# Optimization experiments

Hardware: AMD Instinct MI355X
Metric: run time of the kernel (lower is better)

## Reference

```python
import jax, jax.numpy as jnp
import numpy as np

N_NODES = 100000

def _gcn_norm(edge_index, num_nodes):
    # add self-loops, compute symmetric normalization coeffs per edge
    loops = jnp.arange(num_nodes, dtype=edge_index.dtype)
    src = jnp.concatenate([edge_index[0], loops])
    dst = jnp.concatenate([edge_index[1], loops])
    deg = jax.ops.segment_sum(jnp.ones_like(dst, dtype=jnp.float32), dst,
                              num_segments=num_nodes)
    dinv = jnp.where(deg > 0, jax.lax.rsqrt(deg), 0.0)
    norm = dinv[src] * dinv[dst]  # [E + N]
    return src, dst, norm

def _gcn_conv(x, W, b, src, dst, norm, num_nodes):
    h = x @ W                              # [N, out] transform first (PyG order)
    msg = h[src] * norm[:, None]           # gather + scale
    out = jax.ops.segment_sum(msg, dst, num_segments=num_nodes)  # scatter-add
    return out + b

def setup_inputs() -> dict:
    key = jax.random.key(0)
    k1, k2, k3, k4 = jax.random.split(key, 4)
    F_in, H, C = 128, 64, 40
    x = jax.random.normal(k1, (N_NODES, F_in), dtype=jnp.float32)
    edge_index = jax.random.randint(k2, (2, 1600000), 0, N_NODES, dtype=jnp.int64)
    W1 = jax.random.normal(k3, (F_in, H), dtype=jnp.float32) / np.sqrt(F_in)
    b1 = jnp.zeros((H,), dtype=jnp.float32)
    W2 = jax.random.normal(k4, (H, C), dtype=jnp.float32) / np.sqrt(H)
    b2 = jnp.zeros((C,), dtype=jnp.float32)
    return {"x": x, "edge_index": edge_index, "W1": W1, "b1": b1, "W2": W2, "b2": b2}

def reference(x, edge_index, W1, b1, W2, b2):
    num_nodes = x.shape[0]
    src, dst, norm = _gcn_norm(edge_index, num_nodes)
    h = _gcn_conv(x, W1, b1, src, dst, norm, num_nodes)
    h = jax.nn.relu(h)
    # dropout is identity in eval mode (training=False)
    h = _gcn_conv(h, W2, b2, src, dst, norm, num_nodes)
    return jax.nn.log_softmax(h, axis=1)
```

## Files before the change

kernel.cpp:

```cpp
#include <hip/hip_runtime.h>
#include <math.h>

#define NPB 256
#define BSH 8
#define MAXNB 400
#define BIN_CHUNK 8192
#define HIST_CHUNK 16384

typedef __attribute__((ext_vector_type(8))) short bf16x8;
typedef __attribute__((ext_vector_type(4))) float f32x4;
typedef __attribute__((ext_vector_type(2))) float f32x2;

__device__ __forceinline__ unsigned short f2bf(float f){
  unsigned int u = __float_as_uint(f);
  unsigned int r = (u + 0x7FFFu + ((u >> 16) & 1u)) >> 16;
  return (unsigned short)r;
}

__device__ __forceinline__ bf16x8 cvt8(float4 a, float4 b){
  union { unsigned u[4]; bf16x8 v; } r;
  asm("v_cvt_pk_bf16_f32 %0, %1, %2" : "=v"(r.u[0]) : "v"(a.x), "v"(a.y));
  asm("v_cvt_pk_bf16_f32 %0, %1, %2" : "=v"(r.u[1]) : "v"(a.z), "v"(a.w));
  asm("v_cvt_pk_bf16_f32 %0, %1, %2" : "=v"(r.u[2]) : "v"(b.x), "v"(b.y));
  asm("v_cvt_pk_bf16_f32 %0, %1, %2" : "=v"(r.u[3]) : "v"(b.z), "v"(b.w));
  return r.v;
}

__global__ void k_prep(const float* __restrict__ W1, const float* __restrict__ W2,
                       unsigned short* __restrict__ w1t, unsigned short* __restrict__ w2t,
                       int* __restrict__ bcnt, int NB){
  int t = threadIdx.x;
  if(blockIdx.x == 0){
    for(int i = t; i < 8192; i += 256){
      int k = i >> 6, f = i & 63;
      w1t[f*128 + k] = f2bf(W1[i]);
    }
  } else {
    for(int i = t; i < 3072; i += 256){
      int c = i >> 6, k = i & 63;
      w2t[c*64 + k] = (c < 40) ? f2bf(W2[k*40 + c]) : (unsigned short)0;
    }
    for(int i = t; i < NB; i += 256) bcnt[i] = 0;
  }
}


__global__ __launch_bounds__(256) void k_bhist(const int* __restrict__ dst, int E,
                                               int* __restrict__ bcnt, int NB){
  __shared__ int l[MAXNB];
  int t = threadIdx.x;
  int base = blockIdx.x*HIST_CHUNK;
  int end = base + HIST_CHUNK; if(end > E) end = E;
  for(int b = t; b < NB; b += 256) l[b] = 0;
  __syncthreads();
  for(int i = base + t; i < end; i += 256) atomicAdd(&l[dst[i] >> BSH], 1);
  __syncthreads();
  for(int b = t; b < NB; b += 256){ int c = l[b]; if(c) atomicAdd(&bcnt[b], c); }
}

__global__ void k_bscan(const int* __restrict__ bcnt, int* __restrict__ bofs,
                        int* __restrict__ bcur, int NB, int E){
  __shared__ int sh[1024];
  int t = threadIdx.x;
  int c0 = (2*t   < NB) ? bcnt[2*t]   : 0;
  int c1 = (2*t+1 < NB) ? bcnt[2*t+1] : 0;
  sh[t] = c0 + c1; __syncthreads();
  for(int off = 1; off < 1024; off <<= 1){
    int v = (t >= off) ? sh[t - off] : 0;
    __syncthreads();
    sh[t] += v;
    __syncthreads();
  }
  int pairEx = sh[t] - (c0 + c1);
  if(2*t   < NB){ bofs[2*t]   = pairEx;      bcur[2*t]   = pairEx; }
  if(2*t+1 < NB){ bofs[2*t+1] = pairEx + c0; bcur[2*t+1] = pairEx + c0; }
  if(t == 0) bofs[NB] = E;
}

__global__ __launch_bounds__(256) void k_binpass(const int* __restrict__ src,
                          const int* __restrict__ dst, int E,
                          int* __restrict__ bcur, unsigned int* __restrict__ binned, int NB){
  __shared__ int lcnt[MAXNB];
  __shared__ int lpos[MAXNB];
  int t = threadIdx.x;
  int base = blockIdx.x * BIN_CHUNK;
  int end = base + BIN_CHUNK; if(end > E) end = E;
  for(int b = t; b < NB; b += 256) lcnt[b] = 0;
  __syncthreads();
  for(int i = base + t; i < end; i += 256)
    atomicAdd(&lcnt[dst[i] >> BSH], 1);
  __syncthreads();
  for(int b = t; b < NB; b += 256){
    int c = lcnt[b];
    lpos[b] = c ? atomicAdd(&bcur[b], c) : 0;
  }
  __syncthreads();
  for(int i = base + t; i < end; i += 256){
    int d = dst[i];
    int b = d >> BSH;
    unsigned int rec = (unsigned int)src[i] | ((unsigned int)(d & (NPB-1)) << 17);
    int p = atomicAdd(&lpos[b], 1);
    binned[p] = rec;
  }
}

__global__ __launch_bounds__(256) void k_bscatter(const unsigned int* __restrict__ binned,
     const int* __restrict__ bofs, int* __restrict__ csr, int* __restrict__ row_ofs,
     float* __restrict__ dinv, int N, int E, int NB){
  __shared__ int lcnt[NPB];
  __shared__ int lofs[NPB];
  __shared__ int lcur[NPB];
  __shared__ int wsum[4];
  int b = blockIdx.x, t = threadIdx.x;
  int beg = bofs[b], end = bofs[b+1];
  lcnt[t] = 0;
  __syncthreads();
  for(int i = beg + t; i < end; i += 256) atomicAdd(&lcnt[binned[i] >> 17], 1);
  __syncthreads();
  int c = lcnt[t];
  int lane = t & 63, wid = t >> 6;
  int v = c;
  #pragma unroll
  for(int off = 1; off < 64; off <<= 1){
    int nv = __shfl_up(v, off, 64);
    if(lane >= off) v += nv;
  }
  if(lane == 63) wsum[wid] = v;
  __syncthreads();
  int wpre = 0;
  #pragma unroll
  for(int k2 = 0; k2 < 4; k2++) if(k2 < wid) wpre += wsum[k2];
  int ex = wpre + v - c;
  lofs[t] = beg + ex; lcur[t] = 0;
  int node = (b << BSH) + t;
  if(node < N){
    row_ofs[node] = beg + ex;
    dinv[node] = rsqrtf((float)(c + 1));
  }
  __syncthreads();
  for(int i = beg + t; i < end; i += 256){
    unsigned int rec = binned[i];
    int dl = rec >> 17;
    int pos = lofs[dl] + atomicAdd(&lcur[dl], 1);
    csr[pos] = (int)(rec & 0x1FFFFu);
  }
  if(b == NB-1 && t == 0) row_ofs[N] = E;
}

__global__ __launch_bounds__(256) void k_gemm1(const float* __restrict__ x,
                        const unsigned short* __restrict__ w1t,
                        const float* __restrict__ dinv, unsigned int* __restrict__ g1, int n){
  __shared__ unsigned short xs[128*136];
  __shared__ unsigned short wt[64*136];
  int tid = threadIdx.x;
  int nodeBase = blockIdx.x*128;
  for(int i = tid; i < 1024; i += 256){
    int f = i >> 4, seg = i & 15;
    *(uint4*)&wt[f*136 + seg*8] = *(const uint4*)&w1t[f*128 + seg*8];
  }
  {
    const float4* x4 = (const float4*)x;
    for(int i = tid; i < 2048; i += 256){
      int node = i >> 4, seg = i & 15;
      float4 va = make_float4(0.f,0.f,0.f,0.f), vb = va;
      if(nodeBase + node < n){
        va = x4[(size_t)(nodeBase + node)*32 + seg*2];
        vb = x4[(size_t)(nodeBase + node)*32 + seg*2 + 1];
      }
      *(bf16x8*)&xs[node*136 + seg*8] = cvt8(va, vb);
    }
  }
  __syncthreads();

  int w = tid >> 6, lane = tid & 63;
  int ml = lane & 15, q = lane >> 4;
  int n0 = nodeBase + w*32 + ml;
  int n1 = n0 + 16;
  bool vn0 = n0 < n, vn1 = n1 < n;

  f32x4 a00 = {0.f,0.f,0.f,0.f}, a01 = {0.f,0.f,0.f,0.f},
        a02 = {0.f,0.f,0.f,0.f}, a03 = {0.f,0.f,0.f,0.f};
  f32x4 a10 = {0.f,0.f,0.f,0.f}, a11 = {0.f,0.f,0.f,0.f},
        a12 = {0.f,0.f,0.f,0.f}, a13 = {0.f,0.f,0.f,0.f};
  const unsigned short* brow = &xs[(w*32 + ml)*136 + q*8];
  const unsigned short* arow = &wt[ml*136 + q*8];
  #pragma unroll
  for(int s = 0; s < 4; s++){
    bf16x8 bb0 = *(const bf16x8*)(brow +        s*32);
    bf16x8 bb1 = *(const bf16x8*)(brow + 2176 + s*32);
    bf16x8 a0 = *(const bf16x8*)(arow +    0 + s*32);
    bf16x8 a1 = *(const bf16x8*)(arow + 2176 + s*32);
    bf16x8 a2 = *(const bf16x8*)(arow + 4352 + s*32);
    bf16x8 a3 = *(const bf16x8*)(arow + 6528 + s*32);
    a00 = __builtin_amdgcn_mfma_f32_16x16x32_bf16(a0, bb0, a00, 0, 0, 0);
    a01 = __builtin_amdgcn_mfma_f32_16x16x32_bf16(a1, bb0, a01, 0, 0, 0);
    a02 = __builtin_amdgcn_mfma_f32_16x16x32_bf16(a2, bb0, a02, 0, 0, 0);
    a03 = __builtin_amdgcn_mfma_f32_16x16x32_bf16(a3, bb0, a03, 0, 0, 0);
    a10 = __builtin_amdgcn_mfma_f32_16x16x32_bf16(a0, bb1, a10, 0, 0, 0);
    a11 = __builtin_amdgcn_mfma_f32_16x16x32_bf16(a1, bb1, a11, 0, 0, 0);
    a12 = __builtin_amdgcn_mfma_f32_16x16x32_bf16(a2, bb1, a12, 0, 0, 0);
    a13 = __builtin_amdgcn_mfma_f32_16x16x32_bf16(a3, bb1, a13, 0, 0, 0);
  }
  if(vn0){
    float dv = dinv[n0];
    unsigned base16 = ((unsigned)n0 << 4) + q;
    int p;
    p = __builtin_amdgcn_cvt_pk_fp8_f32(a00[0]*dv, a00[1]*dv, 0, false);
    p = __builtin_amdgcn_cvt_pk_fp8_f32(a00[2]*dv, a00[3]*dv, p, true);
    g1[base16 +  0] = (unsigned)p;
    p = __builtin_amdgcn_cvt_pk_fp8_f32(a01[0]*dv, a01[1]*dv, 0, false);
    p = __builtin_amdgcn_cvt_pk_fp8_f32(a01[2]*dv, a01[3]*dv, p, true);
    g1[base16 +  4] = (unsigned)p;
    p = __builtin_amdgcn_cvt_pk_fp8_f32(a02[0]*dv, a02[1]*dv, 0, false);
    p = __builtin_amdgcn_cvt_pk_fp8_f32(a02[2]*dv, a02[3]*dv, p, true);
    g1[base16 +  8] = (unsigned)p;
    p = __builtin_amdgcn_cvt_pk_fp8_f32(a03[0]*dv, a03[1]*dv, 0, false);
    p = __builtin_amdgcn_cvt_pk_fp8_f32(a03[2]*dv, a03[3]*dv, p, true);
    g1[base16 + 12] = (unsigned)p;
  }
  if(vn1){
    float dv = dinv[n1];
    unsigned base16 = ((unsigned)n1 << 4) + q;
    int p;
    p = __builtin_amdgcn_cvt_pk_fp8_f32(a10[0]*dv, a10[1]*dv, 0, false);
    p = __builtin_amdgcn_cvt_pk_fp8_f32(a10[2]*dv, a10[3]*dv, p, true);
    g1[base16 +  0] = (unsigned)p;
    p = __builtin_amdgcn_cvt_pk_fp8_f32(a11[0]*dv, a11[1]*dv, 0, false);
    p = __builtin_amdgcn_cvt_pk_fp8_f32(a11[2]*dv, a11[3]*dv, p, true);
    g1[base16 +  4] = (unsigned)p;
    p = __builtin_amdgcn_cvt_pk_fp8_f32(a12[0]*dv, a12[1]*dv, 0, false);
    p = __builtin_amdgcn_cvt_pk_fp8_f32(a12[2]*dv, a12[3]*dv, p, true);
    g1[base16 +  8] = (unsigned)p;
    p = __builtin_amdgcn_cvt_pk_fp8_f32(a13[0]*dv, a13[1]*dv, 0, false);
    p = __builtin_amdgcn_cvt_pk_fp8_f32(a13[2]*dv, a13[3]*dv, p, true);
    g1[base16 + 12] = (unsigned)p;
  }
}

__global__ __launch_bounds__(256) void k_agg1g2(const unsigned* __restrict__ g1,
    const int* __restrict__ row_ofs, const int* __restrict__ csr,
    const float* __restrict__ dinv, const float* __restrict__ b1,
    const unsigned short* __restrict__ w2t, unsigned char* __restrict__ g2, int n){
  __shared__ unsigned short us[64*72];
  __shared__ unsigned short ws2[48*72];
  int t = threadIdx.x;
  int nodeBase = blockIdx.x*64;
  for(int i = t; i < 384; i += 256){
    int row = i >> 3, seg = i & 7;
    *(uint4*)&ws2[row*72 + seg*8] = *(const uint4*)&w2t[row*64 + seg*8];
  }
  int lane = t & 63;
  int f = lane & 15;
  int bq = (lane & 48) << 2;
  int qg = t >> 4;
  float4 bb1 = ((const float4*)b1)[f];
  #pragma unroll 1
  for(int i = 0; i < 4; i++){
    int node = nodeBase + qg*4 + i;
    int lrow = qg*4 + i;
    if(node < n){
      int beg = row_ofs[node], end = row_ofs[node+1];
      unsigned v = g1[((unsigned)node << 4) + f];
      f32x2 s01 = __builtin_amdgcn_cvt_pk_f32_fp8(v, false);
      f32x2 s23 = __builtin_amdgcn_cvt_pk_f32_fp8(v, true);
      for(int e = beg; e < end; e += 16){
        int rem = end - e; if(rem > 16) rem = 16;
        int idxv = (f < rem) ? csr[e + f] : 0;
        int j = 0;
        for(; j + 4 <= rem; j += 4){
          int r0 = __builtin_amdgcn_ds_bpermute(bq + ((j+0) << 2), idxv);
          int r1 = __builtin_amdgcn_ds_bpermute(bq + ((j+1) << 2), idxv);
          int r2 = __builtin_amdgcn_ds_bpermute(bq + ((j+2) << 2), idxv);
          int r3 = __builtin_amdgcn_ds_bpermute(bq + ((j+3) << 2), idxv);
          unsigned v0 = g1[((unsigned)r0 << 4) + f];
          unsigned v1 = g1[((unsigned)r1 << 4) + f];
          unsigned v2 = g1[((unsigned)r2 << 4) + f];
          unsigned v3 = g1[((unsigned)r3 << 4) + f];
          s01 += __builtin_amdgcn_cvt_pk_f32_fp8(v0, false);
          s23 += __builtin_amdgcn_cvt_pk_f32_fp8(v0, true);
          s01 += __builtin_amdgcn_cvt_pk_f32_fp8(v1, false);
          s23 += __builtin_amdgcn_cvt_pk_f32_fp8(v1, true);
          s01 += __builtin_amdgcn_cvt_pk_f32_fp8(v2, false);
          s23 += __builtin_amdgcn_cvt_pk_f32_fp8(v2, true);
          s01 += __builtin_amdgcn_cvt_pk_f32_fp8(v3, false);
          s23 += __builtin_amdgcn_cvt_pk_f32_fp8(v3, true);
        }
        for(; j < rem; j++){
          int r0 = __builtin_amdgcn_ds_bpermute(bq + (j << 2), idxv);
          unsigned v0 = g1[((unsigned)r0 << 4) + f];
          s01 += __builtin_amdgcn_cvt_pk_f32_fp8(v0, false);
          s23 += __builtin_amdgcn_cvt_pk_f32_fp8(v0, true);
        }
      }
      float dv = dinv[node];
      float h0 = fmaxf(fmaf(dv, s01.x, bb1.x), 0.f);
      float h1 = fmaxf(fmaf(dv, s01.y, bb1.y), 0.f);
      float h2 = fmaxf(fmaf(dv, s23.x, bb1.z), 0.f);
      float h3 = fmaxf(fmaf(dv, s23.y, bb1.w), 0.f);
      unsigned p0, p1;
      asm("v_cvt_pk_bf16_f32 %0, %1, %2" : "=v"(p0) : "v"(dv*h0), "v"(dv*h1));
      asm("v_cvt_pk_bf16_f32 %0, %1, %2" : "=v"(p1) : "v"(dv*h2), "v"(dv*h3));
      *(uint2*)&us[lrow*72 + f*4] = make_uint2(p0, p1);
    } else {
      *(uint2*)&us[lrow*72 + f*4] = make_uint2(0u, 0u);
    }
  }
  __syncthreads();
  int w = t >> 6;
  int ml = lane & 15, q = lane >> 4;
  f32x4 acc0 = {0.f,0.f,0.f,0.f}, acc1 = {0.f,0.f,0.f,0.f}, acc2 = {0.f,0.f,0.f,0.f};
  const unsigned short* brow = &us[(w*16 + ml)*72 + q*8];
  const unsigned short* a0r = &ws2[ml*72 + q*8];
  #pragma unroll
  for(int s = 0; s < 2; s++){
    bf16x8 bb = *(const bf16x8*)(brow + s*32);
    bf16x8 a0 = *(const bf16x8*)(a0r +    0 + s*32);
    bf16x8 a1 = *(const bf16x8*)(a0r + 1152 + s*32);
    bf16x8 a2 = *(const bf16x8*)(a0r + 2304 + s*32);
    acc0 = __builtin_amdgcn_mfma_f32_16x16x32_bf16(a0, bb, acc0, 0, 0, 0);
    acc1 = __builtin_amdgcn_mfma_f32_16x16x32_bf16(a1, bb, acc1, 0, 0, 0);
    acc2 = __builtin_amdgcn_mfma_f32_16x16x32_bf16(a2, bb, acc2, 0, 0, 0);
  }
  int node = nodeBase + w*16 + ml;
  if(node < n){
    unsigned* gd = (unsigned*)g2;
    unsigned rb = (unsigned)node*10u + q;
    int p;
    p = __builtin_amdgcn_cvt_pk_fp8_f32(acc0[0], acc0[1], 0, false);
    p = __builtin_amdgcn_cvt_pk_fp8_f32(acc0[2], acc0[3], p, true);
    gd[rb + 0] = (unsigned)p;
    p = __builtin_amdgcn_cvt_pk_fp8_f32(acc1[0], acc1[1], 0, false);
    p = __builtin_amdgcn_cvt_pk_fp8_f32(acc1[2], acc1[3], p, true);
    gd[rb + 4] = (unsigned)p;
    if(q < 2){
      p = __builtin_amdgcn_cvt_pk_fp8_f32(acc2[0], acc2[1], 0, false);
      p = __builtin_amdgcn_cvt_pk_fp8_f32(acc2[2], acc2[3], p, true);
      gd[rb + 8] = (unsigned)p;
    }
  }
}

__global__ __launch_bounds__(256) void k_agg2(const unsigned char* __restrict__ g2,
     const int* __restrict__ row_ofs, const int* __restrict__ csr,
     const float* __restrict__ dinv, const float* __restrict__ b2,
     float* __restrict__ out, int N){
  int t = threadIdx.x;
  int lane = t & 63;
  int f = lane & 15;
  int fc = (f < 10) ? f : 0;
  int bq = (lane & 48) << 2;
  int node = blockIdx.x*16 + (t >> 4);
  if(node >= N) return;
  int beg = row_ofs[node], end = row_ofs[node+1];
  const unsigned* gd = (const unsigned*)g2;
  unsigned v = gd[(unsigned)node*10u + fc];
  f32x2 s01 = __builtin_amdgcn_cvt_pk_f32_fp8(v, false);
  f32x2 s23 = __builtin_amdgcn_cvt_pk_f32_fp8(v, true);
  for(int e = beg; e < end; e += 16){
    int rem = end - e; if(rem > 16) rem = 16;
    int idxv = (f < rem) ? csr[e + f] : 0;
    int j = 0;
    for(; j + 4 <= rem; j += 4){
      int r0 = __builtin_amdgcn_ds_bpermute(bq + ((j+0) << 2), idxv);
      int r1 = __builtin_amdgcn_ds_bpermute(bq + ((j+1) << 2), idxv);
      int r2 = __builtin_amdgcn_ds_bpermute(bq + ((j+2) << 2), idxv);
      int r3 = __builtin_amdgcn_ds_bpermute(bq + ((j+3) << 2), idxv);
      unsigned v0 = gd[(unsigned)r0*10u + fc];
      unsigned v1 = gd[(unsigned)r1*10u + fc];
      unsigned v2 = gd[(unsigned)r2*10u + fc];
      unsigned v3 = gd[(unsigned)r3*10u + fc];
      s01 += __builtin_amdgcn_cvt_pk_f32_fp8(v0, false);
      s23 += __builtin_amdgcn_cvt_pk_f32_fp8(v0, true);
      s01 += __builtin_amdgcn_cvt_pk_f32_fp8(v1, false);
      s23 += __builtin_amdgcn_cvt_pk_f32_fp8(v1, true);
      s01 += __builtin_amdgcn_cvt_pk_f32_fp8(v2, false);
      s23 += __builtin_amdgcn_cvt_pk_f32_fp8(v2, true);
      s01 += __builtin_amdgcn_cvt_pk_f32_fp8(v3, false);
      s23 += __builtin_amdgcn_cvt_pk_f32_fp8(v3, true);
    }
    for(; j < rem; j++){
      int r0 = __builtin_amdgcn_ds_bpermute(bq + (j << 2), idxv);
      unsigned v0 = gd[(unsigned)r0*10u + fc];
      s01 += __builtin_amdgcn_cvt_pk_f32_fp8(v0, false);
      s23 += __builtin_amdgcn_cvt_pk_f32_fp8(v0, true);
    }
  }
  float dv = dinv[node];
  float4 bb = ((const float4*)b2)[fc];
  float l0 = fmaf(dv, s01.x, bb.x);
  float l1 = fmaf(dv, s01.y, bb.y);
  float l2 = fmaf(dv, s23.x, bb.z);
  float l3 = fmaf(dv, s23.y, bb.w);
  bool valid = (f < 10);
  float m = valid ? fmaxf(fmaxf(l0,l1), fmaxf(l2,l3)) : -INFINITY;
  m = fmaxf(m, __shfl_xor(m,1,64)); m = fmaxf(m, __shfl_xor(m,2,64));
  m = fmaxf(m, __shfl_xor(m,4,64)); m = fmaxf(m, __shfl_xor(m,8,64));
  float ex = valid ? (expf(l0-m)+expf(l1-m)) + (expf(l2-m)+expf(l3-m)) : 0.f;
  ex += __shfl_xor(ex,1,64); ex += __shfl_xor(ex,2,64);
  ex += __shfl_xor(ex,4,64); ex += __shfl_xor(ex,8,64);
  float ll = logf(ex);
  if(valid){
    ((float4*)out)[(unsigned)node*10u + f] = make_float4(l0-m-ll, l1-m-ll, l2-m-ll, l3-m-ll);
  }
}


extern "C" void kernel_launch(void* const* d_in, const int* in_sizes, int n_in,
                              void* d_out, int out_size, void* d_ws, size_t ws_size,
                              hipStream_t stream){
  const float* x  = (const float*)d_in[0];
  const int*   ei = (const int*)  d_in[1];
  const float* W1 = (const float*)d_in[2];
  const float* b1 = (const float*)d_in[3];
  const float* W2 = (const float*)d_in[4];
  const float* b2 = (const float*)d_in[5];
  float* out = (float*)d_out;

  int N = in_sizes[0] / 128;
  int E = in_sizes[1] / 2;
  const int* src = ei;
  const int* dst = ei + E;
  int NB = (N + NPB - 1) >> BSH;

  char* w = (char*)d_ws;
  auto alloc = [&](size_t bytes) -> char* {
    char* p = w;
    w += (bytes + 511) & ~(size_t)511;
    return p;
  };
  int*   bcnt    = (int*)  alloc((size_t)NB*4);
  int*   bofs    = (int*)  alloc((size_t)(NB+1)*4);
  int*   bcur    = (int*)  alloc((size_t)NB*4);
  int*   row_ofs = (int*)  alloc((size_t)(N+1)*4);
  float* dinv    = (float*)alloc((size_t)N*4);
  unsigned int* binned = (unsigned int*)alloc((size_t)E*4);
  int*   csr     = (int*)  alloc((size_t)E*4);
  unsigned int*   g1 = (unsigned int*)  alloc((size_t)N*64);
  unsigned char*  g2 = (unsigned char*) alloc((size_t)N*40);
  unsigned short* w1t = (unsigned short*)alloc((size_t)64*128*2);
  unsigned short* w2t = (unsigned short*)alloc((size_t)48*64*2);

  k_prep    <<<2, 256, 0, stream>>>(W1, W2, w1t, w2t, bcnt, NB);
  k_bhist   <<<(E+HIST_CHUNK-1)/HIST_CHUNK, 256, 0, stream>>>(dst, E, bcnt, NB);
  k_bscan   <<<1, 1024, 0, stream>>>(bcnt, bofs, bcur, NB, E);
  k_binpass <<<(E+BIN_CHUNK-1)/BIN_CHUNK, 256, 0, stream>>>(src, dst, E, bcur, binned, NB);
  k_bscatter<<<NB, 256, 0, stream>>>(binned, bofs, csr, row_ofs, dinv, N, E, NB);

  k_gemm1   <<<(N+127)/128, 256, 0, stream>>>(x, w1t, dinv, g1, N);
  k_agg1g2  <<<(N+63)/64, 256, 0, stream>>>(g1, row_ofs, csr, dinv, b1, w2t, g2, N);
  k_agg2    <<<(N+15)/16, 256, 0, stream>>>(g2, row_ofs, csr, dinv, b2, out, N);
}
```

Before: 228.1 us.

## Gather 8-byte feature chunks with half-wave per node and padded zero sentinel rows

Both aggregation kernels now give each node 8 lanes, each loading 8 fp8 features as a uint2, instead of 16 lanes loading 4 bytes each. Each wave therefore covers twice as many nodes and issues wider, fewer gather loads. Layer-2 features are padded to 64-byte rows, and a zeroed sentinel row at index N lets out-of-range edge slots load harmlessly, which removes the remainder loops. The prep kernel is folded into the histogram launch and replaced by a memset, and the histogram and binning chunk sizes are reduced so more blocks run. The padding increases layer-2 gather bytes, and the fixed 8-wide inner loop does wasted loads on low-degree nodes.

```diff
diff --git a/kernel.cpp b/kernel.cpp
--- a/kernel.cpp
+++ b/kernel.cpp
@@ -4,8 +4,8 @@
 #define NPB 256
 #define BSH 8
 #define MAXNB 400
-#define BIN_CHUNK 8192
-#define HIST_CHUNK 16384
+#define BIN_CHUNK 4096
+#define HIST_CHUNK 4096
 
 typedef __attribute__((ext_vector_type(8))) short bf16x8;
 typedef __attribute__((ext_vector_type(4))) float f32x4;
@@ -26,36 +26,40 @@
   return r.v;
 }
 
-__global__ void k_prep(const float* __restrict__ W1, const float* __restrict__ W2,
-                       unsigned short* __restrict__ w1t, unsigned short* __restrict__ w2t,
-                       int* __restrict__ bcnt, int NB){
-  int t = threadIdx.x;
-  if(blockIdx.x == 0){
-    for(int i = t; i < 8192; i += 256){
-      int k = i >> 6, f = i & 63;
-      w1t[f*128 + k] = f2bf(W1[i]);
-    }
-  } else {
-    for(int i = t; i < 3072; i += 256){
-      int c = i >> 6, k = i & 63;
-      w2t[c*64 + k] = (c < 40) ? f2bf(W2[k*40 + c]) : (unsigned short)0;
-    }
-    for(int i = t; i < NB; i += 256) bcnt[i] = 0;
-  }
-}
-
 
 __global__ __launch_bounds__(256) void k_bhist(const int* __restrict__ dst, int E,
-                                               int* __restrict__ bcnt, int NB){
+                                               int* __restrict__ bcnt, int NB, int NBH,
+                                               const float* __restrict__ W1,
+                                               const float* __restrict__ W2,
+                                               unsigned short* __restrict__ w1t,
+                                               unsigned short* __restrict__ w2t,
+                                               unsigned* __restrict__ g1,
+                                               unsigned* __restrict__ g2d, int N){
   __shared__ int l[MAXNB];
-  int t = threadIdx.x;
-  int base = blockIdx.x*HIST_CHUNK;
+  int t = threadIdx.x, b = blockIdx.x;
+  if(b >= NBH){
+    if(b == NBH){
+      for(int i = t; i < 8192; i += 256){
+        int k = i >> 6, f = i & 63;
+        w1t[f*128 + k] = f2bf(W1[i]);
+      }
+      if(t < 16) g1[((size_t)(unsigned)N << 4) + t] = 0;
+    } else {
+      for(int i = t; i < 3072; i += 256){
+        int c = i >> 6, k = i & 63;
+        w2t[c*64 + k] = (c < 40) ? f2bf(W2[k*40 + c]) : (unsigned short)0;
+      }
+      if(t < 16) g2d[((size_t)(unsigned)N << 4) + t] = 0;
+    }
+    return;
+  }
+  int base = b*HIST_CHUNK;
   int end = base + HIST_CHUNK; if(end > E) end = E;
-  for(int b = t; b < NB; b += 256) l[b] = 0;
+  for(int i = t; i < NB; i += 256) l[i] = 0;
   __syncthreads();
   for(int i = base + t; i < end; i += 256) atomicAdd(&l[dst[i] >> BSH], 1);
   __syncthreads();
-  for(int b = t; b < NB; b += 256){ int c = l[b]; if(c) atomicAdd(&bcnt[b], c); }
+  for(int i = t; i < NB; i += 256){ int c = l[i]; if(c) atomicAdd(&bcnt[i], c); }
 }
 
 __global__ void k_bscan(const int* __restrict__ bcnt, int* __restrict__ bofs,
@@ -237,10 +241,16 @@
   }
 }
 
+#define ACC8(W) { \
+  s0 += __builtin_amdgcn_cvt_pk_f32_fp8(W.x, false); \
+  s1 += __builtin_amdgcn_cvt_pk_f32_fp8(W.x, true);  \
+  s2 += __builtin_amdgcn_cvt_pk_f32_fp8(W.y, false); \
+  s3 += __builtin_amdgcn_cvt_pk_f32_fp8(W.y, true); }
+
 __global__ __launch_bounds__(256) void k_agg1g2(const unsigned* __restrict__ g1,
     const int* __restrict__ row_ofs, const int* __restrict__ csr,
     const float* __restrict__ dinv, const float* __restrict__ b1,
-    const unsigned short* __restrict__ w2t, unsigned char* __restrict__ g2, int n){
+    const unsigned short* __restrict__ w2t, unsigned* __restrict__ g2d, int n){
   __shared__ unsigned short us[64*72];
   __shared__ unsigned short ws2[48*72];
   int t = threadIdx.x;
@@ -250,60 +260,65 @@
     *(uint4*)&ws2[row*72 + seg*8] = *(const uint4*)&w2t[row*64 + seg*8];
   }
   int lane = t & 63;
-  int f = lane & 15;
-  int bq = (lane & 48) << 2;
+  int hl = lane & 7;
+  int half = (lane >> 3) & 1;
+  int bqh = ((lane & 48) << 2) + half*32;
   int qg = t >> 4;
-  float4 bb1 = ((const float4*)b1)[f];
+  const char* g1c = (const char*)g1;
+  float4 b1a = ((const float4*)b1)[hl*2];
+  float4 b1b = ((const float4*)b1)[hl*2+1];
   #pragma unroll 1
-  for(int i = 0; i < 4; i++){
-    int node = nodeBase + qg*4 + i;
-    int lrow = qg*4 + i;
+  for(int p = 0; p < 2; p++){
+    int lrow = qg*4 + p*2 + half;
+    int node = nodeBase + lrow;
+    f32x2 s0={0.f,0.f}, s1={0.f,0.f}, s2={0.f,0.f}, s3={0.f,0.f};
+    int e = 0, end = 0; float dv = 0.f;
     if(node < n){
-      int beg = row_ofs[node], end = row_ofs[node+1];
-      unsigned v = g1[((unsigned)node << 4) + f];
-      f32x2 s01 = __builtin_amdgcn_cvt_pk_f32_fp8(v, false);
-      f32x2 s23 = __builtin_amdgcn_cvt_pk_f32_fp8(v, true);
-      for(int e = beg; e < end; e += 16){
-        int rem = end - e; if(rem > 16) rem = 16;
-        int idxv = (f < rem) ? csr[e + f] : 0;
-        int j = 0;
-        for(; j + 4 <= rem; j += 4){
-          int r0 = __builtin_amdgcn_ds_bpermute(bq + ((j+0) << 2), idxv);
-          int r1 = __builtin_amdgcn_ds_bpermute(bq + ((j+1) << 2), idxv);
-          int r2 = __builtin_amdgcn_ds_bpermute(bq + ((j+2) << 2), idxv);
-          int r3 = __builtin_amdgcn_ds_bpermute(bq + ((j+3) << 2), idxv);
-          unsigned v0 = g1[((unsigned)r0 << 4) + f];
-          unsigned v1 = g1[((unsigned)r1 << 4) + f];
-          unsigned v2 = g1[((unsigned)r2 << 4) + f];
-          unsigned v3 = g1[((unsigned)r3 << 4) + f];
-          s01 += __builtin_amdgcn_cvt_pk_f32_fp8(v0, false);
-          s23 += __builtin_amdgcn_cvt_pk_f32_fp8(v0, true);
-          s01 += __builtin_amdgcn_cvt_pk_f32_fp8(v1, false);
-          s23 += __builtin_amdgcn_cvt_pk_f32_fp8(v1, true);
-          s01 += __builtin_amdgcn_cvt_pk_f32_fp8(v2, false);
-          s23 += __builtin_amdgcn_cvt_pk_f32_fp8(v2, true);
-          s01 += __builtin_amdgcn_cvt_pk_f32_fp8(v3, false);
-          s23 += __builtin_amdgcn_cvt_pk_f32_fp8(v3, true);
-        }
-        for(; j < rem; j++){
-          int r0 = __builtin_amdgcn_ds_bpermute(bq + (j << 2), idxv);
-          unsigned v0 = g1[((unsigned)r0 << 4) + f];
-          s01 += __builtin_amdgcn_cvt_pk_f32_fp8(v0, false);
-          s23 += __builtin_amdgcn_cvt_pk_f32_fp8(v0, true);
-        }
-      }
-      float dv = dinv[node];
-      float h0 = fmaxf(fmaf(dv, s01.x, bb1.x), 0.f);
-      float h1 = fmaxf(fmaf(dv, s01.y, bb1.y), 0.f);
-      float h2 = fmaxf(fmaf(dv, s23.x, bb1.z), 0.f);
-      float h3 = fmaxf(fmaf(dv, s23.y, bb1.w), 0.f);
-      unsigned p0, p1;
+      e = row_ofs[node]; end = row_ofs[node+1];
+      dv = dinv[node];
+      uint2 sv = *(const uint2*)(g1c + ((size_t)(unsigned)node << 6) + (hl<<3));
+      s0 = __builtin_amdgcn_cvt_pk_f32_fp8(sv.x, false);
+      s1 = __builtin_amdgcn_cvt_pk_f32_fp8(sv.x, true);
+      s2 = __builtin_amdgcn_cvt_pk_f32_fp8(sv.y, false);
+      s3 = __builtin_amdgcn_cvt_pk_f32_fp8(sv.y, true);
+    }
+    for(; e < end; e += 8){
+      int idxv = (e + hl < end) ? csr[e + hl] : n;
+      int r0 = __builtin_amdgcn_ds_bpermute(bqh +  0, idxv);
+      int r1 = __builtin_amdgcn_ds_bpermute(bqh +  4, idxv);
+      int r2 = __builtin_amdgcn_ds_bpermute(bqh +  8, idxv);
+      int r3 = __builtin_amdgcn_ds_bpermute(bqh + 12, idxv);
+      int r4 = __builtin_amdgcn_ds_bpermute(bqh + 16, idxv);
+      int r5 = __builtin_amdgcn_ds_bpermute(bqh + 20, idxv);
+      int r6 = __builtin_amdgcn_ds_bpermute(bqh + 24, idxv);
+      int r7 = __builtin_amdgcn_ds_bpermute(bqh + 28, idxv);
+      uint2 w0 = *(const uint2*)(g1c + ((size_t)(unsigned)r0 << 6) + (hl<<3));
+      uint2 w1 = *(const uint2*)(g1c + ((size_t)(unsigned)r1 << 6) + (hl<<3));
+      uint2 w2 = *(const uint2*)(g1c + ((size_t)(unsigned)r2 << 6) + (hl<<3));
+      uint2 w3 = *(const uint2*)(g1c + ((size_t)(unsigned)r3 << 6) + (hl<<3));
+      uint2 w4 = *(const uint2*)(g1c + ((size_t)(unsigned)r4 << 6) + (hl<<3));
+      uint2 w5 = *(const uint2*)(g1c + ((size_t)(unsigned)r5 << 6) + (hl<<3));
+      uint2 w6 = *(const uint2*)(g1c + ((size_t)(unsigned)r6 << 6) + (hl<<3));
+      uint2 w7 = *(const uint2*)(g1c + ((size_t)(unsigned)r7 << 6) + (hl<<3));
+      ACC8(w0); ACC8(w1); ACC8(w2); ACC8(w3);
+      ACC8(w4); ACC8(w5); ACC8(w6); ACC8(w7);
+    }
+    unsigned p0 = 0, p1 = 0, p2 = 0, p3 = 0;
+    if(node < n){
+      float h0 = fmaxf(fmaf(dv, s0.x, b1a.x), 0.f);
+      float h1 = fmaxf(fmaf(dv, s0.y, b1a.y), 0.f);
+      float h2 = fmaxf(fmaf(dv, s1.x, b1a.z), 0.f);
+      float h3 = fmaxf(fmaf(dv, s1.y, b1a.w), 0.f);
+      float h4 = fmaxf(fmaf(dv, s2.x, b1b.x), 0.f);
+      float h5 = fmaxf(fmaf(dv, s2.y, b1b.y), 0.f);
+      float h6 = fmaxf(fmaf(dv, s3.x, b1b.z), 0.f);
+      float h7 = fmaxf(fmaf(dv, s3.y, b1b.w), 0.f);
       asm("v_cvt_pk_bf16_f32 %0, %1, %2" : "=v"(p0) : "v"(dv*h0), "v"(dv*h1));
       asm("v_cvt_pk_bf16_f32 %0, %1, %2" : "=v"(p1) : "v"(dv*h2), "v"(dv*h3));
-      *(uint2*)&us[lrow*72 + f*4] = make_uint2(p0, p1);
-    } else {
-      *(uint2*)&us[lrow*72 + f*4] = make_uint2(0u, 0u);
-    }
+      asm("v_cvt_pk_bf16_f32 %0, %1, %2" : "=v"(p2) : "v"(dv*h4), "v"(dv*h5));
+      asm("v_cvt_pk_bf16_f32 %0, %1, %2" : "=v"(p3) : "v"(dv*h6), "v"(dv*h7));
+    }
+    *(uint4*)&us[lrow*72 + hl*8] = make_uint4(p0, p1, p2, p3);
   }
   __syncthreads();
   int w = t >> 6;
@@ -323,84 +338,94 @@
   }
   int node = nodeBase + w*16 + ml;
   if(node < n){
-    unsigned* gd = (unsigned*)g2;
-    unsigned rb = (unsigned)node*10u + q;
+    unsigned rb = ((unsigned)node << 4) + q;
     int p;
     p = __builtin_amdgcn_cvt_pk_fp8_f32(acc0[0], acc0[1], 0, false);
     p = __builtin_amdgcn_cvt_pk_fp8_f32(acc0[2], acc0[3], p, true);
-    gd[rb + 0] = (unsigned)p;
+    g2d[rb + 0] = (unsigned)p;
     p = __builtin_amdgcn_cvt_pk_fp8_f32(acc1[0], acc1[1], 0, false);
     p = __builtin_amdgcn_cvt_pk_fp8_f32(acc1[2], acc1[3], p, true);
-    gd[rb + 4] = (unsigned)p;
+    g2d[rb + 4] = (unsigned)p;
     if(q < 2){
       p = __builtin_amdgcn_cvt_pk_fp8_f32(acc2[0], acc2[1], 0, false);
       p = __builtin_amdgcn_cvt_pk_fp8_f32(acc2[2], acc2[3], p, true);
-      gd[rb + 8] = (unsigned)p;
-    }
-  }
-}
-
-__global__ __launch_bounds__(256) void k_agg2(const unsigned char* __restrict__ g2,
+      g2d[rb + 8] = (unsigned)p;
+    } else {
+      g2d[rb + 8] = 0;
+    }
+    g2d[rb + 12] = 0;
+  }
+}
+
+__global__ __launch_bounds__(256) void k_agg2(const unsigned* __restrict__ g2d,
      const int* __restrict__ row_ofs, const int* __restrict__ csr,
      const float* __restrict__ dinv, const float* __restrict__ b2,
      float* __restrict__ out, int N){
   int t = threadIdx.x;
   int lane = t & 63;
-  int f = lane & 15;
-  int fc = (f < 10) ? f : 0;
-  int bq = (lane & 48) << 2;
-  int node = blockIdx.x*16 + (t >> 4);
-  if(node >= N) return;
-  int beg = row_ofs[node], end = row_ofs[node+1];
-  const unsigned* gd = (const unsigned*)g2;
-  unsigned v = gd[(unsigned)node*10u + fc];
-  f32x2 s01 = __builtin_amdgcn_cvt_pk_f32_fp8(v, false);
-  f32x2 s23 = __builtin_amdgcn_cvt_pk_f32_fp8(v, true);
-  for(int e = beg; e < end; e += 16){
-    int rem = end - e; if(rem > 16) rem = 16;
-    int idxv = (f < rem) ? csr[e + f] : 0;
-    int j = 0;
-    for(; j + 4 <= rem; j += 4){
-      int r0 = __builtin_amdgcn_ds_bpermute(bq + ((j+0) << 2), idxv);
-      int r1 = __builtin_amdgcn_ds_bpermute(bq + ((j+1) << 2), idxv);
-      int r2 = __builtin_amdgcn_ds_bpermute(bq + ((j+2) << 2), idxv);
-      int r3 = __builtin_amdgcn_ds_bpermute(bq + ((j+3) << 2), idxv);
-      unsigned v0 = gd[(unsigned)r0*10u + fc];
-      unsigned v1 = gd[(unsigned)r1*10u + fc];
-      unsigned v2 = gd[(unsigned)r2*10u + fc];
-      unsigned v3 = gd[(unsigned)r3*10u + fc];
-      s01 += __builtin_amdgcn_cvt_pk_f32_fp8(v0, false);
-      s23 += __builtin_amdgcn_cvt_pk_f32_fp8(v0, true);
-      s01 += __builtin_amdgcn_cvt_pk_f32_fp8(v1, false);
-      s23 += __builtin_amdgcn_cvt_pk_f32_fp8(v1, true);
-      s01 += __builtin_amdgcn_cvt_pk_f32_fp8(v2, false);
-      s23 += __builtin_amdgcn_cvt_pk_f32_fp8(v2, true);
-      s01 += __builtin_amdgcn_cvt_pk_f32_fp8(v3, false);
-      s23 += __builtin_amdgcn_cvt_pk_f32_fp8(v3, true);
-    }
-    for(; j < rem; j++){
-      int r0 = __builtin_amdgcn_ds_bpermute(bq + (j << 2), idxv);
-      unsigned v0 = gd[(unsigned)r0*10u + fc];
-      s01 += __builtin_amdgcn_cvt_pk_f32_fp8(v0, false);
-      s23 += __builtin_amdgcn_cvt_pk_f32_fp8(v0, true);
-    }
-  }
-  float dv = dinv[node];
-  float4 bb = ((const float4*)b2)[fc];
-  float l0 = fmaf(dv, s01.x, bb.x);
-  float l1 = fmaf(dv, s01.y, bb.y);
-  float l2 = fmaf(dv, s23.x, bb.z);
-  float l3 = fmaf(dv, s23.y, bb.w);
-  bool valid = (f < 10);
-  float m = valid ? fmaxf(fmaxf(l0,l1), fmaxf(l2,l3)) : -INFINITY;
+  int hl = lane & 7;
+  int half = (lane >> 3) & 1;
+  int bqh = ((lane & 48) << 2) + half*32;
+  int qg = t >> 4;
+  int node = blockIdx.x*32 + qg*2 + half;
+  const char* g2c = (const char*)g2d;
+  int hc = (hl < 5) ? hl : 0;
+  float4 b2a = ((const float4*)b2)[hc*2];
+  float4 b2b = ((const float4*)b2)[hc*2+1];
+  f32x2 s0={0.f,0.f}, s1={0.f,0.f}, s2={0.f,0.f}, s3={0.f,0.f};
+  int e = 0, end = 0; float dv = 0.f;
+  if(node < N){
+    e = row_ofs[node]; end = row_ofs[node+1];
+    dv = dinv[node];
+    uint2 sv = *(const uint2*)(g2c + ((size_t)(unsigned)node << 6) + (hl<<3));
+    s0 = __builtin_amdgcn_cvt_pk_f32_fp8(sv.x, false);
+    s1 = __builtin_amdgcn_cvt_pk_f32_fp8(sv.x, true);
+    s2 = __builtin_amdgcn_cvt_pk_f32_fp8(sv.y, false);
+    s3 = __builtin_amdgcn_cvt_pk_f32_fp8(sv.y, true);
+  }
+  for(; e < end; e += 8){
+    int idxv = (e + hl < end) ? csr[e + hl] : N;
+    int r0 = __builtin_amdgcn_ds_bpermute(bqh +  0, idxv);
+    int r1 = __builtin_amdgcn_ds_bpermute(bqh +  4, idxv);
+    int r2 = __builtin_amdgcn_ds_bpermute(bqh +  8, idxv);
+    int r3 = __builtin_amdgcn_ds_bpermute(bqh + 12, idxv);
+    int r4 = __builtin_amdgcn_ds_bpermute(bqh + 16, idxv);
+    int r5 = __builtin_amdgcn_ds_bpermute(bqh + 20, idxv);
+    int r6 = __builtin_amdgcn_ds_bpermute(bqh + 24, idxv);
+    int r7 = __builtin_amdgcn_ds_bpermute(bqh + 28, idxv);
+    uint2 w0 = *(const uint2*)(g2c + ((size_t)(unsigned)r0 << 6) + (hl<<3));
+    uint2 w1 = *(const uint2*)(g2c + ((size_t)(unsigned)r1 << 6) + (hl<<3));
+    uint2 w2 = *(const uint2*)(g2c + ((size_t)(unsigned)r2 << 6) + (hl<<3));
+    uint2 w3 = *(const uint2*)(g2c + ((size_t)(unsigned)r3 << 6) + (hl<<3));
+    uint2 w4 = *(const uint2*)(g2c + ((size_t)(unsigned)r4 << 6) + (hl<<3));
+    uint2 w5 = *(const uint2*)(g2c + ((size_t)(unsigned)r5 << 6) + (hl<<3));
+    uint2 w6 = *(const uint2*)(g2c + ((size_t)(unsigned)r6 << 6) + (hl<<3));
+    uint2 w7 = *(const uint2*)(g2c + ((size_t)(unsigned)r7 << 6) + (hl<<3));
+    ACC8(w0); ACC8(w1); ACC8(w2); ACC8(w3);
+    ACC8(w4); ACC8(w5); ACC8(w6); ACC8(w7);
+  }
+  float l0 = fmaf(dv, s0.x, b2a.x);
+  float l1 = fmaf(dv, s0.y, b2a.y);
+  float l2 = fmaf(dv, s1.x, b2a.z);
+  float l3 = fmaf(dv, s1.y, b2a.w);
+  float l4 = fmaf(dv, s2.x, b2b.x);
+  float l5 = fmaf(dv, s2.y, b2b.y);
+  float l6 = fmaf(dv, s3.x, b2b.z);
+  float l7 = fmaf(dv, s3.y, b2b.w);
+  bool valid = (hl < 5);
+  float m = valid ? fmaxf(fmaxf(fmaxf(l0,l1), fmaxf(l2,l3)),
+                          fmaxf(fmaxf(l4,l5), fmaxf(l6,l7))) : -INFINITY;
   m = fmaxf(m, __shfl_xor(m,1,64)); m = fmaxf(m, __shfl_xor(m,2,64));
-  m = fmaxf(m, __shfl_xor(m,4,64)); m = fmaxf(m, __shfl_xor(m,8,64));
-  float ex = valid ? (expf(l0-m)+expf(l1-m)) + (expf(l2-m)+expf(l3-m)) : 0.f;
+  m = fmaxf(m, __shfl_xor(m,4,64));
+  float ex = valid ? ((expf(l0-m)+expf(l1-m)) + (expf(l2-m)+expf(l3-m)))
+                   + ((expf(l4-m)+expf(l5-m)) + (expf(l6-m)+expf(l7-m))) : 0.f;
   ex += __shfl_xor(ex,1,64); ex += __shfl_xor(ex,2,64);
-  ex += __shfl_xor(ex,4,64); ex += __shfl_xor(ex,8,64);
+  ex += __shfl_xor(ex,4,64);
   float ll = logf(ex);
-  if(valid){
-    ((float4*)out)[(unsigned)node*10u + f] = make_float4(l0-m-ll, l1-m-ll, l2-m-ll, l3-m-ll);
+  if(valid && node < N){
+    float4* o4 = (float4*)out;
+    o4[(unsigned)node*10u + hl*2    ] = make_float4(l0-m-ll, l1-m-ll, l2-m-ll, l3-m-ll);
+    o4[(unsigned)node*10u + hl*2 + 1] = make_float4(l4-m-ll, l5-m-ll, l6-m-ll, l7-m-ll);
   }
 }
 
@@ -435,18 +460,20 @@
   float* dinv    = (float*)alloc((size_t)N*4);
   unsigned int* binned = (unsigned int*)alloc((size_t)E*4);
   int*   csr     = (int*)  alloc((size_t)E*4);
-  unsigned int*   g1 = (unsigned int*)  alloc((size_t)N*64);
-  unsigned char*  g2 = (unsigned char*) alloc((size_t)N*40);
+  unsigned int*   g1 = (unsigned int*)  alloc((size_t)(N+1)*64);
+  unsigned int*   g2 = (unsigned int*)  alloc((size_t)(N+1)*64);
   unsigned short* w1t = (unsigned short*)alloc((size_t)64*128*2);
   unsigned short* w2t = (unsigned short*)alloc((size_t)48*64*2);
 
-  k_prep    <<<2, 256, 0, stream>>>(W1, W2, w1t, w2t, bcnt, NB);
-  k_bhist   <<<(E+HIST_CHUNK-1)/HIST_CHUNK, 256, 0, stream>>>(dst, E, bcnt, NB);
+  int NBH = (E + HIST_CHUNK - 1)/HIST_CHUNK;
+
+  hipMemsetAsync(bcnt, 0, (size_t)NB*4, stream);
+  k_bhist   <<<NBH+2, 256, 0, stream>>>(dst, E, bcnt, NB, NBH, W1, W2, w1t, w2t, g1, g2, N);
   k_bscan   <<<1, 1024, 0, stream>>>(bcnt, bofs, bcur, NB, E);
   k_binpass <<<(E+BIN_CHUNK-1)/BIN_CHUNK, 256, 0, stream>>>(src, dst, E, bcur, binned, NB);
   k_bscatter<<<NB, 256, 0, stream>>>(binned, bofs, csr, row_ofs, dinv, N, E, NB);
 
   k_gemm1   <<<(N+127)/128, 256, 0, stream>>>(x, w1t, dinv, g1, N);
   k_agg1g2  <<<(N+63)/64, 256, 0, stream>>>(g1, row_ofs, csr, dinv, b1, w2t, g2, N);
-  k_agg2    <<<(N+15)/16, 256, 0, stream>>>(g2, row_ofs, csr, dinv, b2, out, N);
-}
+  k_agg2    <<<(N+31)/32, 256, 0, stream>>>(g2, row_ofs, csr, dinv, b2, out, N);
+}
```

After: 212.8 us, median of 2. 6.7% less time.
